# Kernel tuning notes

Hardware: AMD Instinct MI355X
Metric: run time of the kernel (lower is better)

The kernel has to match this reference:

```python
import jax, jax.numpy as jnp
import numpy as np

B, S, H, D = 256, 512, 512, 1  # batch, seq_len, rnn_hid_size (== S*D), input_dim


def lstm_cell(x, h, c, Wih, Whh, bih, bhh):
    # torch.nn.LSTMCell: gates ordered i, f, g, o
    g = x @ Wih.T + bih + h @ Whh.T + bhh  # [B, 4H]
    i, f, gg, o = jnp.split(g, 4, axis=-1)
    i = jax.nn.sigmoid(i)
    f = jax.nn.sigmoid(f)
    gg = jnp.tanh(gg)
    o = jax.nn.sigmoid(o)
    c_new = f * c + i * gg
    h_new = o * jnp.tanh(c_new)
    return h_new, c_new


def setup_inputs() -> dict:
    key = jax.random.key(0)
    ks = jax.random.split(key, 14)
    sc = 1.0 / np.sqrt(H)  # torch LSTMCell/Linear default uniform bound
    u = lambda k, shape: jax.random.uniform(k, shape, jnp.float32, -sc, sc)
    values = jax.random.normal(ks[0], (B, S), jnp.float32)
    masks = jax.random.randint(ks[1], (B, S), 0, 2).astype(jnp.float32)
    return {
        "values": values,
        "masks": masks,
        "Wih_f": u(ks[2], (4 * H, D)), "Whh_f": u(ks[3], (4 * H, H)),
        "bih_f": u(ks[4], (4 * H,)), "bhh_f": u(ks[5], (4 * H,)),
        "Wih_b": u(ks[6], (4 * H, D)), "Whh_b": u(ks[7], (4 * H, H)),
        "bih_b": u(ks[8], (4 * H,)), "bhh_b": u(ks[9], (4 * H,)),
        "W_imp": u(ks[10], (D, H)), "b_imp": u(ks[11], (D,)),
    }


def reference(values, masks, Wih_f, Whh_f, bih_f, bhh_f,
              Wih_b, Whh_b, bih_b, bhh_b, W_imp, b_imp):
    x_f = values[:, :, None]  # [B, S, 1]
    m_f = masks[:, :, None]
    # flip over axis 2 (size 1) is a no-op, matching the original exactly
    x_b = jnp.flip(x_f, axis=2)
    m_b = jnp.flip(m_f, axis=2)

    start_f = jnp.full((B, D), 128.0, jnp.float32)
    start_b = jnp.full((B, D), -128.0, jnp.float32)
    z = jnp.zeros((B, H), jnp.float32)
    h_f, c_f = lstm_cell(start_f, z, z, Wih_f, Whh_f, bih_f, bhh_f)
    h_b, c_b = lstm_cell(start_b, z, z, Wih_b, Whh_b, bih_b, bhh_b)

    xs = (jnp.swapaxes(x_f, 0, 1), jnp.swapaxes(m_f, 0, 1),
          jnp.swapaxes(x_b, 0, 1), jnp.swapaxes(m_b, 0, 1))  # [S, B, 1] each

    def step(carry, inp):
        hf, cf, hb, cb = carry
        xf, mf, xb, mb = inp
        imp_f = hf @ W_imp.T + b_imp
        imp_b = hb @ W_imp.T + b_imp
        cc_f = (1.0 - mf) * xf + mf * imp_f
        cc_b = (1.0 - mb) * xb + mb * imp_b
        hf, cf = lstm_cell(cc_f, hf, cf, Wih_f, Whh_f, bih_f, bhh_f)
        hb, cb = lstm_cell(cc_b, hb, cb, Wih_b, Whh_b, bih_b, bhh_b)
        return (hf, cf, hb, cb), None

    (h_f, c_f, h_b, c_b), _ = jax.lax.scan(step, (h_f, c_f, h_b, c_b), xs)
    h = h_f + h_b  # [B, H]
    imputations = h.reshape(B, S, D)  # requires H == S * D
    out = imputations * (1.0 - m_f) + x_f * m_f
    return h, out
```

## Files before the change

kernel.cpp:

```cpp
#include <hip/hip_runtime.h>
#include <stdint.h>

#define B_ 256
#define S_ 512
#define H_ 512

#define XM_STRIDE 513
#define LDS_BYTES 82176

typedef __attribute__((ext_vector_type(4))) float f32x4;
typedef __attribute__((ext_vector_type(4))) int   i32x4;
typedef __attribute__((ext_vector_type(8))) short s16x8;

__device__ __forceinline__ short f2bf(float f) {
    union { float f; uint32_t u; } c; c.f = f;
    uint32_t u = c.u;
    u += 0x7fffu + ((u >> 16) & 1u);
    return (short)(u >> 16);
}
__device__ __forceinline__ float bflo(uint32_t u) { return __builtin_bit_cast(float, u << 16); }
__device__ __forceinline__ float bfhi(uint32_t u) { return __builtin_bit_cast(float, u & 0xffff0000u); }
__device__ __forceinline__ float sig_(float x)  { return 1.0f / (1.0f + __expf(-x)); }
__device__ __forceinline__ float tanh_(float x) { return 1.0f - 2.0f / (1.0f + __expf(2.0f * x)); }

__device__ __forceinline__ void load_a16_issue(const void* p, i32x4* a) {
    asm volatile(
        "global_load_dwordx4 %0, %16, off sc0 sc1\n\t"
        "global_load_dwordx4 %1, %16, off offset:64 sc0 sc1\n\t"
        "global_load_dwordx4 %2, %16, off offset:128 sc0 sc1\n\t"
        "global_load_dwordx4 %3, %16, off offset:192 sc0 sc1\n\t"
        "global_load_dwordx4 %4, %16, off offset:256 sc0 sc1\n\t"
        "global_load_dwordx4 %5, %16, off offset:320 sc0 sc1\n\t"
        "global_load_dwordx4 %6, %16, off offset:384 sc0 sc1\n\t"
        "global_load_dwordx4 %7, %16, off offset:448 sc0 sc1\n\t"
        "global_load_dwordx4 %8, %16, off offset:512 sc0 sc1\n\t"
        "global_load_dwordx4 %9, %16, off offset:576 sc0 sc1\n\t"
        "global_load_dwordx4 %10, %16, off offset:640 sc0 sc1\n\t"
        "global_load_dwordx4 %11, %16, off offset:704 sc0 sc1\n\t"
        "global_load_dwordx4 %12, %16, off offset:768 sc0 sc1\n\t"
        "global_load_dwordx4 %13, %16, off offset:832 sc0 sc1\n\t"
        "global_load_dwordx4 %14, %16, off offset:896 sc0 sc1\n\t"
        "global_load_dwordx4 %15, %16, off offset:960 sc0 sc1"
        : "=v"(a[0]), "=v"(a[1]), "=v"(a[2]), "=v"(a[3]),
          "=v"(a[4]), "=v"(a[5]), "=v"(a[6]), "=v"(a[7]),
          "=v"(a[8]), "=v"(a[9]), "=v"(a[10]), "=v"(a[11]),
          "=v"(a[12]), "=v"(a[13]), "=v"(a[14]), "=v"(a[15])
        : "v"(p)
        : "memory");
}
#define AWAIT(imm, x0, x1, x2, x3) \
    asm volatile("s_waitcnt vmcnt(" #imm ")" : "+v"(x0), "+v"(x1), "+v"(x2), "+v"(x3) :: "memory")

__device__ __forceinline__ void store_h4(void* p, int h0, int h1, int h2, int h3) {
    asm volatile(
        "global_store_short %4, %0, off sc0 sc1\n\t"
        "global_store_short %4, %1, off offset:1024 sc0 sc1\n\t"
        "global_store_short %4, %2, off offset:2048 sc0 sc1\n\t"
        "global_store_short %4, %3, off offset:3072 sc0 sc1"
        :: "v"(h0), "v"(h1), "v"(h2), "v"(h3), "v"(p)
        : "memory");
}

__global__ void __launch_bounds__(256, 1)
lstm_kernel(const float* __restrict__ values, const float* __restrict__ masks,
            const float* __restrict__ Wih_f, const float* __restrict__ Whh_f,
            const float* __restrict__ bih_f, const float* __restrict__ bhh_f,
            const float* __restrict__ Wih_b, const float* __restrict__ Whh_b,
            const float* __restrict__ bih_b, const float* __restrict__ bhh_b,
            const float* __restrict__ W_imp, const float* __restrict__ b_imp,
            unsigned int* ctrs, short* h_buf, float* hfin)
{
    extern __shared__ char smem_raw[];
    short*    imp_lds = (short*)smem_raw;
    uint32_t* xm_lds  = (uint32_t*)(smem_raw + 16384);

    uint32_t* flags = (uint32_t*)ctrs + 64;

    const int tid  = threadIdx.x;
    const int lane = tid & 63;
    const int wave = tid >> 6;
    const int mw = wave >> 1;
    const int nw = wave & 1;

    const int bid = blockIdx.x;
    const int xg  = bid & 7;
    const int s_  = bid >> 3;
    const int d   = s_ & 1;
    const int w   = s_ >> 1;
    const int cluster = xg * 2 + d;

    const float* Whh = d ? Whh_b : Whh_f;
    const float* Wih = d ? Wih_b : Wih_f;
    const float* bih = d ? bih_b : bih_f;
    const float* bhh = d ? bhh_b : bhh_f;

    const int col16 = lane & 15;
    const int koff4 = lane >> 4;
    const int jcol  = w * 32 + nw * 16 + col16;

    for (int c = tid; c < 1024; c += 256) {
        int ckoff = (c >> 4) & 3, ckb = c >> 6;
        int k0 = ckb * 32 + ckoff * 8;
        short* dst = &imp_lds[c * 8];
        #pragma unroll
        for (int j = 0; j < 8; ++j) dst[j] = f2bf(W_imp[k0 + j]);
    }
    for (int i = tid; i < 32 * 512; i += 256) {
        int r = i >> 9, s = i & 511;
        float x = values[(xg * 32 + r) * S_ + s];
        float m = masks[(xg * 32 + r) * S_ + s];
        float a = x * (1.0f - m);
        xm_lds[r * XM_STRIDE + s] =
            (uint32_t)(uint16_t)f2bf(a) | ((uint32_t)(uint16_t)f2bf(m) << 16);
    }

    s16x8 bfr[4][16];
    {
        const float* base = Whh + (size_t)jcol * 512 + koff4 * 8;
        #pragma unroll
        for (int g = 0; g < 4; ++g) {
            const float* src = base + (size_t)g * 512 * 512;
            #pragma unroll
            for (int kb = 0; kb < 16; ++kb) {
                f32x4 v0 = *(const f32x4*)(src + kb * 32);
                f32x4 v1 = *(const f32x4*)(src + kb * 32 + 4);
                s16x8 b;
                b[0] = f2bf(v0[0]); b[1] = f2bf(v0[1]); b[2] = f2bf(v0[2]); b[3] = f2bf(v0[3]);
                b[4] = f2bf(v1[0]); b[5] = f2bf(v1[1]); b[6] = f2bf(v1[2]); b[7] = f2bf(v1[3]);
                bfr[g][kb] = b;
            }
        }
    }

    float bias[4], wih[4];
    #pragma unroll
    for (int g = 0; g < 4; ++g) {
        int gc = g * 512 + jcol;
        bias[g] = bih[gc] + bhh[gc];
        wih[g]  = Wih[gc];
    }
    const float bimp  = b_imp[0];
    const float start = d ? -128.0f : 128.0f;

    const int arow    = xg * 32 + mw * 16 + col16;
    const int rowloc  = mw * 16 + koff4 * 4;
    const int rowbase = xg * 32 + rowloc;
    const int imp_off = (koff4 * 16 + col16) * 8;

    uint32_t*       myflag = flags + cluster * 16 + w;
    const uint32_t* pollp  = flags + cluster * 16 + col16;

    __syncthreads();

    float c_reg[4];
    {
        float pre[4];
        #pragma unroll
        for (int g = 0; g < 4; ++g) pre[g] = start * wih[g] + bias[g];
        float i0 = sig_(pre[0]), g0 = tanh_(pre[2]), o0 = sig_(pre[3]);
        float c0 = i0 * g0;
        float h0 = o0 * tanh_(c0);
        #pragma unroll
        for (int r = 0; r < 4; ++r) c_reg[r] = c0;
        int hb16 = (int)(unsigned short)(unsigned)f2bf(h0);
        short* dst = h_buf + d * (B_ * H_) + (size_t)rowbase * H_ + jcol;
        store_h4(dst, hb16, hb16, hb16, hb16);
    }
    asm volatile("s_waitcnt vmcnt(0)" ::: "memory");
    __syncthreads();
    if (tid == 0)
        asm volatile("global_store_dword %0, %1, off sc0 sc1" :: "v"(myflag), "v"(1u) : "memory");

    for (int t = 0; t < S_; ++t) {
        const int p = t & 1;
        const short* hb_r = h_buf + p       * (2 * B_ * H_) + d * (B_ * H_);
        short*       hb_w = h_buf + (p ^ 1) * (2 * B_ * H_) + d * (B_ * H_);

        if (wave == 0) {
            const uint32_t tgt = (uint32_t)(t + 1);
            for (;;) {
                uint32_t f;
                asm volatile("global_load_dword %0, %1, off sc0 sc1\n\ts_waitcnt vmcnt(0)"
                             : "=v"(f) : "v"(pollp) : "memory");
                if (__ballot(f >= tgt) == ~0ull) break;
                __builtin_amdgcn_s_sleep(2);
            }
        }
        __syncthreads();

        i32x4 a_regs[16];
        load_a16_issue(hb_r + (size_t)arow * H_ + koff4 * 8, a_regs);

        f32x4 acc0 = {0,0,0,0}, acc1 = {0,0,0,0}, acc2 = {0,0,0,0}, acc3 = {0,0,0,0};
        f32x4 acc4 = {0,0,0,0};
        AWAIT(12, a_regs[0], a_regs[1], a_regs[2], a_regs[3]);
        #pragma unroll
        for (int kb = 0; kb < 4; ++kb) {
            s16x8 a = __builtin_bit_cast(s16x8, a_regs[kb]);
            acc0 = __builtin_amdgcn_mfma_f32_16x16x32_bf16(a, bfr[0][kb], acc0, 0, 0, 0);
            acc1 = __builtin_amdgcn_mfma_f32_16x16x32_bf16(a, bfr[1][kb], acc1, 0, 0, 0);
            acc2 = __builtin_amdgcn_mfma_f32_16x16x32_bf16(a, bfr[2][kb], acc2, 0, 0, 0);
            acc3 = __builtin_amdgcn_mfma_f32_16x16x32_bf16(a, bfr[3][kb], acc3, 0, 0, 0);
            s16x8 b4 = *(const s16x8*)&imp_lds[kb * 512 + imp_off];
            acc4 = __builtin_amdgcn_mfma_f32_16x16x32_bf16(a, b4, acc4, 0, 0, 0);
        }
        AWAIT(8, a_regs[4], a_regs[5], a_regs[6], a_regs[7]);
        #pragma unroll
        for (int kb = 4; kb < 8; ++kb) {
            s16x8 a = __builtin_bit_cast(s16x8, a_regs[kb]);
            acc0 = __builtin_amdgcn_mfma_f32_16x16x32_bf16(a, bfr[0][kb], acc0, 0, 0, 0);
            acc1 = __builtin_amdgcn_mfma_f32_16x16x32_bf16(a, bfr[1][kb], acc1, 0, 0, 0);
            acc2 = __builtin_amdgcn_mfma_f32_16x16x32_bf16(a, bfr[2][kb], acc2, 0, 0, 0);
            acc3 = __builtin_amdgcn_mfma_f32_16x16x32_bf16(a, bfr[3][kb], acc3, 0, 0, 0);
            s16x8 b4 = *(const s16x8*)&imp_lds[kb * 512 + imp_off];
            acc4 = __builtin_amdgcn_mfma_f32_16x16x32_bf16(a, b4, acc4, 0, 0, 0);
        }
        AWAIT(4, a_regs[8], a_regs[9], a_regs[10], a_regs[11]);
        #pragma unroll
        for (int kb = 8; kb < 12; ++kb) {
            s16x8 a = __builtin_bit_cast(s16x8, a_regs[kb]);
            acc0 = __builtin_amdgcn_mfma_f32_16x16x32_bf16(a, bfr[0][kb], acc0, 0, 0, 0);
            acc1 = __builtin_amdgcn_mfma_f32_16x16x32_bf16(a, bfr[1][kb], acc1, 0, 0, 0);
            acc2 = __builtin_amdgcn_mfma_f32_16x16x32_bf16(a, bfr[2][kb], acc2, 0, 0, 0);
            acc3 = __builtin_amdgcn_mfma_f32_16x16x32_bf16(a, bfr[3][kb], acc3, 0, 0, 0);
            s16x8 b4 = *(const s16x8*)&imp_lds[kb * 512 + imp_off];
            acc4 = __builtin_amdgcn_mfma_f32_16x16x32_bf16(a, b4, acc4, 0, 0, 0);
        }
        AWAIT(0, a_regs[12], a_regs[13], a_regs[14], a_regs[15]);
        #pragma unroll
        for (int kb = 12; kb < 16; ++kb) {
            s16x8 a = __builtin_bit_cast(s16x8, a_regs[kb]);
            acc0 = __builtin_amdgcn_mfma_f32_16x16x32_bf16(a, bfr[0][kb], acc0, 0, 0, 0);
            acc1 = __builtin_amdgcn_mfma_f32_16x16x32_bf16(a, bfr[1][kb], acc1, 0, 0, 0);
            acc2 = __builtin_amdgcn_mfma_f32_16x16x32_bf16(a, bfr[2][kb], acc2, 0, 0, 0);
            acc3 = __builtin_amdgcn_mfma_f32_16x16x32_bf16(a, bfr[3][kb], acc3, 0, 0, 0);
            s16x8 b4 = *(const s16x8*)&imp_lds[kb * 512 + imp_off];
            acc4 = __builtin_amdgcn_mfma_f32_16x16x32_bf16(a, b4, acc4, 0, 0, 0);
        }

        int hbits[4];
        #pragma unroll
        for (int r = 0; r < 4; ++r) {
            uint32_t pk = xm_lds[(rowloc + r) * XM_STRIDE + t];
            float cc = bflo(pk) + bfhi(pk) * (acc4[r] + bimp);
            float pi = acc0[r] + cc * wih[0] + bias[0];
            float pf = acc1[r] + cc * wih[1] + bias[1];
            float pg = acc2[r] + cc * wih[2] + bias[2];
            float po = acc3[r] + cc * wih[3] + bias[3];
            float iv = sig_(pi), fv = sig_(pf), gv = tanh_(pg), ov = sig_(po);
            c_reg[r] = fv * c_reg[r] + iv * gv;
            float hn = ov * tanh_(c_reg[r]);
            hbits[r] = (int)(unsigned short)(unsigned)f2bf(hn);
            if (t == S_ - 1) hfin[d * (B_ * H_) + (rowbase + r) * H_ + jcol] = hn;
        }
        store_h4(hb_w + (size_t)rowbase * H_ + jcol, hbits[0], hbits[1], hbits[2], hbits[3]);

        asm volatile("s_waitcnt vmcnt(0)" ::: "memory");
        __syncthreads();
        if (tid == 0)
            asm volatile("global_store_dword %0, %1, off sc0 sc1"
                         :: "v"(myflag), "v"((uint32_t)(t + 2)) : "memory");
    }
}

__global__ void __launch_bounds__(256)
epilogue_kernel(const float* __restrict__ values, const float* __restrict__ masks,
                const float* __restrict__ hfin, float* __restrict__ out)
{
    int i = blockIdx.x * 256 + threadIdx.x;
    float h = hfin[i] + hfin[B_ * H_ + i];
    out[i] = h;
    float xv = values[i], mv = masks[i];
    out[B_ * H_ + i] = h * (1.0f - mv) + xv * mv;
}

extern "C" void kernel_launch(void* const* d_in, const int* in_sizes, int n_in,
                              void* d_out, int out_size, void* d_ws, size_t ws_size,
                              hipStream_t stream) {
    const float* values = (const float*)d_in[0];
    const float* masks  = (const float*)d_in[1];
    const float* Wih_f  = (const float*)d_in[2];
    const float* Whh_f  = (const float*)d_in[3];
    const float* bih_f  = (const float*)d_in[4];
    const float* bhh_f  = (const float*)d_in[5];
    const float* Wih_b  = (const float*)d_in[6];
    const float* Whh_b  = (const float*)d_in[7];
    const float* bih_b  = (const float*)d_in[8];
    const float* bhh_b  = (const float*)d_in[9];
    const float* W_imp  = (const float*)d_in[10];
    const float* b_imp  = (const float*)d_in[11];

    unsigned int* ctrs = (unsigned int*)d_ws;
    short* h_buf = (short*)((char*)d_ws + 8192);
    float* hfin  = (float*)((char*)d_ws + 8192 + 2 * 2 * B_ * H_ * sizeof(short));

    hipMemsetAsync(d_ws, 0, 8192, stream);

    hipFuncSetAttribute((const void*)lstm_kernel,
                        hipFuncAttributeMaxDynamicSharedMemorySize, LDS_BYTES);

    void* args[] = {
        (void*)&values, (void*)&masks,
        (void*)&Wih_f, (void*)&Whh_f, (void*)&bih_f, (void*)&bhh_f,
        (void*)&Wih_b, (void*)&Whh_b, (void*)&bih_b, (void*)&bhh_b,
        (void*)&W_imp, (void*)&b_imp,
        (void*)&ctrs, (void*)&h_buf, (void*)&hfin
    };
    hipError_t err = hipLaunchCooperativeKernel((const void*)lstm_kernel,
                                                dim3(256), dim3(256), args,
                                                (unsigned int)LDS_BYTES, stream);
    if (err != hipSuccess) {
        lstm_kernel<<<dim3(256), dim3(256), LDS_BYTES, stream>>>(
            values, masks, Wih_f, Whh_f, bih_f, bhh_f,
            Wih_b, Whh_b, bih_b, bhh_b, W_imp, b_imp, ctrs, h_buf, hfin);
    }

    epilogue_kernel<<<dim3((B_ * H_) / 256), dim3(256), 0, stream>>>(
        values, masks, hfin, (float*)d_out);
}
```

Measured before the change: 2.736 ms.

## Split LSTM recurrence into 512 two-wave blocks of 16 batch rows

Changes the work decomposition of the persistent cooperative LSTM kernel. Before, 256 blocks of 4 waves each covered 32 batch rows. Now 512 blocks of 2 waves each cover 16 rows, giving 32 sync clusters instead of 16, and LDS per block shrinks to match. The aim is finer-grained blocks whose per-step intra-block barrier couples fewer waves, which may spread better across CUs. In exchange there are twice as many flag-polling clusters, and the Whh bf16 register slice is replicated across more blocks.

```diff
diff --git a/kernel.cpp b/kernel.cpp
--- a/kernel.cpp
+++ b/kernel.cpp
@@ -6,7 +6,7 @@
 #define H_ 512
 
 #define XM_STRIDE 513
-#define LDS_BYTES 82176
+#define LDS_BYTES 56320
 
 typedef __attribute__((ext_vector_type(4))) float f32x4;
 typedef __attribute__((ext_vector_type(4))) int   i32x4;
@@ -61,7 +61,7 @@
         : "memory");
 }
 
-__global__ void __launch_bounds__(256, 1)
+__global__ void __launch_bounds__(128, 1)
 lstm_kernel(const float* __restrict__ values, const float* __restrict__ masks,
             const float* __restrict__ Wih_f, const float* __restrict__ Whh_f,
             const float* __restrict__ bih_f, const float* __restrict__ bhh_f,
@@ -79,15 +79,13 @@
     const int tid  = threadIdx.x;
     const int lane = tid & 63;
     const int wave = tid >> 6;
-    const int mw = wave >> 1;
-    const int nw = wave & 1;
+    const int nw = wave;
 
     const int bid = blockIdx.x;
-    const int xg  = bid & 7;
-    const int s_  = bid >> 3;
-    const int d   = s_ & 1;
-    const int w   = s_ >> 1;
-    const int cluster = xg * 2 + d;
+    const int g   = bid & 15;
+    const int w   = (bid >> 4) & 15;
+    const int d   = bid >> 8;
+    const int cluster = d * 16 + g;
 
     const float* Whh = d ? Whh_b : Whh_f;
     const float* Wih = d ? Wih_b : Wih_f;
@@ -98,17 +96,17 @@
     const int koff4 = lane >> 4;
     const int jcol  = w * 32 + nw * 16 + col16;
 
-    for (int c = tid; c < 1024; c += 256) {
+    for (int c = tid; c < 1024; c += 128) {
         int ckoff = (c >> 4) & 3, ckb = c >> 6;
         int k0 = ckb * 32 + ckoff * 8;
         short* dst = &imp_lds[c * 8];
         #pragma unroll
         for (int j = 0; j < 8; ++j) dst[j] = f2bf(W_imp[k0 + j]);
     }
-    for (int i = tid; i < 32 * 512; i += 256) {
+    for (int i = tid; i < 16 * 512; i += 128) {
         int r = i >> 9, s = i & 511;
-        float x = values[(xg * 32 + r) * S_ + s];
-        float m = masks[(xg * 32 + r) * S_ + s];
+        float x = values[(g * 16 + r) * S_ + s];
+        float m = masks[(g * 16 + r) * S_ + s];
         float a = x * (1.0f - m);
         xm_lds[r * XM_STRIDE + s] =
             (uint32_t)(uint16_t)f2bf(a) | ((uint32_t)(uint16_t)f2bf(m) << 16);
@@ -118,8 +116,8 @@
     {
         const float* base = Whh + (size_t)jcol * 512 + koff4 * 8;
         #pragma unroll
-        for (int g = 0; g < 4; ++g) {
-            const float* src = base + (size_t)g * 512 * 512;
+        for (int gg = 0; gg < 4; ++gg) {
+            const float* src = base + (size_t)gg * 512 * 512;
             #pragma unroll
             for (int kb = 0; kb < 16; ++kb) {
                 f32x4 v0 = *(const f32x4*)(src + kb * 32);
@@ -127,24 +125,24 @@
                 s16x8 b;
                 b[0] = f2bf(v0[0]); b[1] = f2bf(v0[1]); b[2] = f2bf(v0[2]); b[3] = f2bf(v0[3]);
                 b[4] = f2bf(v1[0]); b[5] = f2bf(v1[1]); b[6] = f2bf(v1[2]); b[7] = f2bf(v1[3]);
-                bfr[g][kb] = b;
+                bfr[gg][kb] = b;
             }
         }
     }
 
     float bias[4], wih[4];
     #pragma unroll
-    for (int g = 0; g < 4; ++g) {
-        int gc = g * 512 + jcol;
-        bias[g] = bih[gc] + bhh[gc];
-        wih[g]  = Wih[gc];
+    for (int gg = 0; gg < 4; ++gg) {
+        int gc = gg * 512 + jcol;
+        bias[gg] = bih[gc] + bhh[gc];
+        wih[gg]  = Wih[gc];
     }
     const float bimp  = b_imp[0];
     const float start = d ? -128.0f : 128.0f;
 
-    const int arow    = xg * 32 + mw * 16 + col16;
-    const int rowloc  = mw * 16 + koff4 * 4;
-    const int rowbase = xg * 32 + rowloc;
+    const int arow    = g * 16 + col16;
+    const int rowloc  = koff4 * 4;
+    const int rowbase = g * 16 + rowloc;
     const int imp_off = (koff4 * 16 + col16) * 8;
 
     uint32_t*       myflag = flags + cluster * 16 + w;
@@ -156,7 +154,7 @@
     {
         float pre[4];
         #pragma unroll
-        for (int g = 0; g < 4; ++g) pre[g] = start * wih[g] + bias[g];
+        for (int gg = 0; gg < 4; ++gg) pre[gg] = start * wih[gg] + bias[gg];
         float i0 = sig_(pre[0]), g0 = tanh_(pre[2]), o0 = sig_(pre[3]);
         float c0 = i0 * g0;
         float h0 = o0 * tanh_(c0);
@@ -307,10 +305,10 @@
         (void*)&ctrs, (void*)&h_buf, (void*)&hfin
     };
     hipError_t err = hipLaunchCooperativeKernel((const void*)lstm_kernel,
-                                                dim3(256), dim3(256), args,
+                                                dim3(512), dim3(128), args,
                                                 (unsigned int)LDS_BYTES, stream);
     if (err != hipSuccess) {
-        lstm_kernel<<<dim3(256), dim3(256), LDS_BYTES, stream>>>(
+        lstm_kernel<<<dim3(512), dim3(128), LDS_BYTES, stream>>>(
             values, masks, Wih_f, Whh_f, bih_f, bhh_f,
             Wih_b, Whh_b, bih_b, bhh_b, W_imp, b_imp, ctrs, h_buf, hfin);
     }
```

Result: faster. 2.309 ms (-15.6%).
